# Kernel optimization log

Hardware: AMD Instinct MI355X
Metric: run time of the kernel (lower is better)

The kernel has to match this reference:

```python
import jax, jax.numpy as jnp
import numpy as np

MAX_DEG = 10
DEG_COUNTS = [10000, 130000, 170000, 160000, 100000, 15000, 5000, 2500, 2500, 2500, 2500]
DEG_STARTS = [int(s) for s in np.concatenate([[0], np.cumsum(DEG_COUNTS)[:-1]])]
N_ATOMS = int(sum(DEG_COUNTS))
BATCH = 24000
N_TASKS = 12
IN_FEAT = 75
CHANNELS = [IN_FEAT, 15, 20, 27, 36]


def setup_inputs() -> dict:
    key = jax.random.key(0)
    ks = jax.random.split(key, 32)
    inp = {}
    inp['atom_features'] = jax.random.normal(ks[0], (N_ATOMS, IN_FEAT), dtype=jnp.float32)
    # degree_slice[d] = (start, count) of atoms of degree d (atoms are sorted by degree)
    inp['degree_slice'] = jnp.array(np.stack([DEG_STARTS, DEG_COUNTS], axis=1), dtype=jnp.int32)
    inp['membership'] = jax.random.randint(ks[1], (N_ATOMS,), 0, BATCH, dtype=jnp.int32)
    for d in range(1, MAX_DEG + 1):
        inp[f'deg_adj_{d}'] = jax.random.randint(ks[1 + d], (DEG_COUNTS[d], d), 0, N_ATOMS, dtype=jnp.int32)
    for i in range(4):
        fi, fo = CHANNELS[i], CHANNELS[i + 1]
        inp[f'W{i+1}'] = (jax.random.normal(ks[12 + 2 * i], (2 * MAX_DEG + 1, fi, fo), dtype=jnp.float32)
                          / np.float32(np.sqrt(fi)))
        inp[f'b{i+1}'] = jnp.zeros((2 * MAX_DEG + 1, fo), dtype=jnp.float32)
    inp['W_dense'] = jax.random.normal(ks[30], (2 * CHANNELS[-1], N_TASKS * 2), dtype=jnp.float32) / np.float32(np.sqrt(2 * CHANNELS[-1]))
    inp['b_dense'] = jnp.zeros((N_TASKS * 2,), dtype=jnp.float32)
    return inp


def graph_conv(atoms, deg_adjs, W, b):
    # W: [2*MAX_DEG+1, in, out]; weight iterator order: (rel_d, self_d) for d=1..MAX_DEG, then self_0
    outs = [None] * (MAX_DEG + 1)
    for deg in range(1, MAX_DEG + 1):
        adj = deg_adjs[deg - 1]                      # [n_d, deg] neighbor indices
        rel = jnp.sum(atoms[adj], axis=1)            # gather + sum over neighbors -> [n_d, in]
        s, c = DEG_STARTS[deg], DEG_COUNTS[deg]
        self_atoms = atoms[s:s + c]                  # atoms of this degree (static slice)
        i = 2 * (deg - 1)
        outs[deg] = (rel @ W[i] + b[i]) + (self_atoms @ W[i + 1] + b[i + 1])
    outs[0] = atoms[:DEG_COUNTS[0]] @ W[2 * MAX_DEG] + b[2 * MAX_DEG]
    return jax.nn.selu(jnp.concatenate(outs, axis=0))


def graph_gather(atoms, membership):
    sums = jax.ops.segment_sum(atoms, membership, num_segments=BATCH)
    maxs = jax.ops.segment_max(atoms, membership, num_segments=BATCH)
    return jnp.tanh(jnp.concatenate([sums, maxs], axis=1))  # [BATCH, 2*36]


def reference(atom_features, degree_slice, membership,
              deg_adj_1, deg_adj_2, deg_adj_3, deg_adj_4, deg_adj_5,
              deg_adj_6, deg_adj_7, deg_adj_8, deg_adj_9, deg_adj_10,
              W1, b1, W2, b2, W3, b3, W4, b4, W_dense, b_dense):
    # degree_slice carries the same (start,count) info as the static DEG_STARTS/DEG_COUNTS.
    deg_adjs = [deg_adj_1, deg_adj_2, deg_adj_3, deg_adj_4, deg_adj_5,
                deg_adj_6, deg_adj_7, deg_adj_8, deg_adj_9, deg_adj_10]
    x = graph_conv(atom_features, deg_adjs, W1, b1)
    x = graph_conv(x, deg_adjs, W2, b2)
    x = graph_conv(x, deg_adjs, W3, b3)
    x = graph_conv(x, deg_adjs, W4, b4)
    mol = graph_gather(x, membership)                 # [BATCH, 72]
    logits = (mol @ W_dense + b_dense).reshape(BATCH, N_TASKS, 2)
    return jax.nn.softmax(logits, axis=-1)
```

## Files before the change

### kernel.cpp

```cpp
#include <hip/hip_runtime.h>
#include <hip/hip_fp16.h>
#include <cstdint>

#define NT 256
#define PT 128
#define N_ATOMS_C 600000
#define BATCH_C 24000

constexpr int K_COUNTS[11] = {10000,130000,170000,160000,100000,15000,5000,2500,2500,2500,2500};
constexpr int K_STARTS[11] = {0,10000,140000,310000,470000,570000,585000,590000,592500,595000,597500};
constexpr int DORD[11] = {10,9,8,7,6,5,4,3,2,1,0};

struct AdjPtrs { const int* p[10]; };

typedef _Float16 f16x8 __attribute__((ext_vector_type(8)));
typedef float f32x4 __attribute__((ext_vector_type(4)));

__device__ __forceinline__ float selu_f(float x) {
    const float scale = 1.0507009873554805f;
    const float alpha = 1.6732632423543772f;
    return scale * (x > 0.f ? x : alpha * expm1f(x));
}

__device__ __forceinline__ float2 up2(unsigned u) {
    const __half2 h = __builtin_bit_cast(__half2, u);
    return __half22float2(h);
}
__device__ __forceinline__ unsigned pack2(float a, float b) {
    const __half2 h = __float22half2_rn(make_float2(a, b));
    return __builtin_bit_cast(unsigned, h);
}

template<int NLD4>
__device__ __forceinline__ void load_row(const uint2* __restrict__ p, float* r) {
#pragma unroll
    for (int v = 0; v < NLD4; ++v) {
        const uint2 t = p[v];
        const float2 a = up2(t.x), b = up2(t.y);
        r[4*v] = a.x; r[4*v+1] = a.y; r[4*v+2] = b.x; r[4*v+3] = b.y;
    }
}
template<int NLD4>
__device__ __forceinline__ void add_row(const uint2* __restrict__ p, float* r) {
#pragma unroll
    for (int v = 0; v < NLD4; ++v) {
        const uint2 t = p[v];
        const float2 a = up2(t.x), b = up2(t.y);
        r[4*v] += a.x; r[4*v+1] += a.y; r[4*v+2] += b.x; r[4*v+3] += b.y;
    }
}
template<int NF, int FO>
__device__ __forceinline__ void fma_strip(const float* r, const float* __restrict__ w,
                                          float* acc) {
#pragma unroll
    for (int f = 0; f < NF; ++f)
#pragma unroll
        for (int o = 0; o < FO; ++o)
            acc[o] = fmaf(r[f], w[f * FO + o], acc[o]);
}

template<int TB>
__device__ __forceinline__ void blk2degT(int blk, int& deg, int& s, int& cnt, int& tile) {
    deg = 0; s = 0; cnt = 0; tile = 0;
#pragma unroll
    for (int di = 0; di < 11; ++di) {
        const int d = DORD[di];
        const int nb = (K_COUNTS[d] + TB - 1) / TB;
        if (blk < nb) { deg = d; s = K_STARTS[d]; cnt = K_COUNTS[d]; tile = blk; return; }
        blk -= nb;
    }
}

__global__ __launch_bounds__(128) void prep_kernel(
    const float* __restrict__ x0,
    const float* __restrict__ W,
    const float* __restrict__ bias,
    const int* __restrict__ mem,
    int* __restrict__ cnt,
    unsigned short* __restrict__ z,
    unsigned short* __restrict__ srow)
{
    __shared__ _Float16 sx[PT * 104];
    __shared__ _Float16 sb[80 * 104];

    int deg, s, c, tile;
    blk2degT<PT>(blockIdx.x, deg, s, c, tile);
    const int a0 = tile * PT;
    const int na = min(PT, c - a0);
    const int tid = threadIdx.x;
    const int wi_b = deg ? (2 * deg - 1) : 20;

    const float* src = x0 + (size_t)(s + a0) * 75;
    for (int i = tid; i < na * 75; i += PT) {
        const int j = i / 75, f = i - j * 75;
        sx[j * 104 + f] = (_Float16)src[i];
    }
    for (int i = tid; i < PT * 29; i += PT) {
        const int j = i / 29, f = 75 + (i - j * 29);
        sx[j * 104 + f] = (_Float16)0.f;
    }
    for (int i = tid; i < 80 * 104; i += PT) {
        const int col = i / 104, k = i - col * 104;
        const int p = col >> 4, o = col & 15;
        const int wi = (p < 4) ? 2 * p : wi_b;
        const float v = (k < 75 && o < 15) ? W[wi * 1125 + k * 15 + o] : 0.f;
        sb[col * 104 + k] = (_Float16)v;
    }
    __syncthreads();

    if (tid < na) atomicAdd(&cnt[mem[s + a0 + tid]], 1);

    const int lane = tid & 63, w = tid >> 6;
    const int lrow = lane & 15;
    const int kgrp = (lane >> 4) * 8;
    const int row0 = (lane >> 4) * 4;
    const int colo = lane & 15;

    float badd = 0.f;
    if (colo < 15)
        badd = bias[wi_b * 15 + colo] + (deg ? bias[2 * (deg - 1) * 15 + colo] : 0.f);

    f16x8 af[4][3];
#pragma unroll
    for (int mt = 0; mt < 4; ++mt)
#pragma unroll
        for (int ks = 0; ks < 3; ++ks)
            af[mt][ks] = *(const f16x8*)&sx[(w * 64 + mt * 16 + lrow) * 104 + ks * 32 + kgrp];

#pragma unroll
    for (int nt = 0; nt < 5; ++nt) {
        f16x8 bf[3];
#pragma unroll
        for (int ks = 0; ks < 3; ++ks)
            bf[ks] = *(const f16x8*)&sb[(nt * 16 + lrow) * 104 + ks * 32 + kgrp];
#pragma unroll
        for (int mt = 0; mt < 4; ++mt) {
            f32x4 acc = {0.f, 0.f, 0.f, 0.f};
#pragma unroll
            for (int ks = 0; ks < 3; ++ks)
                acc = __builtin_amdgcn_mfma_f32_16x16x32_f16(af[mt][ks], bf[ks], acc, 0, 0, 0);
#pragma unroll
            for (int reg = 0; reg < 4; ++reg) {
                const int ar = w * 64 + mt * 16 + row0 + reg;
                if (ar < na) {
                    const size_t atom = (size_t)(s + a0 + ar);
                    if (nt < 4) {
                        z[(size_t)nt * ((size_t)N_ATOMS_C * 16) + atom * 16 + colo] =
                            __builtin_bit_cast(unsigned short, (_Float16)acc[reg]);
                    } else {
                        const float v = (colo < 15) ? acc[reg] + badd : 0.f;
                        srow[atom * 16 + colo] =
                            __builtin_bit_cast(unsigned short, (_Float16)v);
                    }
                }
            }
        }
    }
}

__global__ __launch_bounds__(256) void conv1_kernel(
    const float* __restrict__ x0,
    const unsigned short* __restrict__ z,
    const unsigned short* __restrict__ srow,
    const float* __restrict__ W,
    AdjPtrs adjp,
    unsigned short* __restrict__ y1)
{
    int deg, s, c, tile;
    blk2degT<NT>(blockIdx.x, deg, s, c, tile);
    const int a = tile * NT + threadIdx.x;
    if (a >= c) return;
    const int atom = s + a;

    float acc[15];
    {
        const uint2* sp = reinterpret_cast<const uint2*>(srow + (size_t)atom * 16);
        float r[16];
        load_row<4>(sp, r);
#pragma unroll
        for (int o = 0; o < 15; ++o) acc[o] = r[o];
    }

    if (deg >= 1 && deg <= 4) {
        const unsigned short* zd = z + (size_t)(deg - 1) * ((size_t)N_ATOMS_C * 16);
        const int* ad = adjp.p[deg - 1] + (size_t)a * deg;
        int nb[4];
#pragma unroll
        for (int k = 0; k < 4; ++k) nb[k] = ad[k < deg ? k : 0];
        uint4 t[4][2];
#pragma unroll
        for (int k = 0; k < 4; ++k) {
            const uint4* p = reinterpret_cast<const uint4*>(zd + (size_t)nb[k] * 16);
            t[k][0] = p[0]; t[k][1] = p[1];
        }
#pragma unroll
        for (int k = 0; k < 4; ++k) {
            if (k < deg) {
                const unsigned w[8] = {t[k][0].x, t[k][0].y, t[k][0].z, t[k][0].w,
                                       t[k][1].x, t[k][1].y, t[k][1].z, t[k][1].w};
#pragma unroll
                for (int v = 0; v < 8; ++v) {
                    const float2 lo = up2(w[v]);
                    if (2 * v < 15)     acc[2 * v]     += lo.x;
                    if (2 * v + 1 < 15) acc[2 * v + 1] += lo.y;
                }
            }
        }
    } else if (deg >= 5) {
        const float* Wa = W + 2 * (deg - 1) * 1125;
        const int* ad = adjp.p[deg - 1] + (size_t)a * deg;
#pragma unroll 1
        for (int st = 0; st < 3; ++st) {
            float r[25];
#pragma unroll
            for (int j = 0; j < 25; ++j) r[j] = 0.f;
            for (int k = 0; k < deg; ++k) {
                const float* xr = x0 + (size_t)ad[k] * 75 + st * 25;
#pragma unroll
                for (int j = 0; j < 25; ++j) r[j] += xr[j];
            }
            fma_strip<25, 15>(r, Wa + st * 25 * 15, acc);
        }
    }

    uint2* yp = reinterpret_cast<uint2*>(y1 + (size_t)atom * 16);
    float o_[16];
#pragma unroll
    for (int o = 0; o < 16; ++o) o_[o] = (o < 15) ? selu_f(acc[o]) : 0.f;
    yp[0] = make_uint2(pack2(o_[0],o_[1]),  pack2(o_[2],o_[3]));
    yp[1] = make_uint2(pack2(o_[4],o_[5]),  pack2(o_[6],o_[7]));
    yp[2] = make_uint2(pack2(o_[8],o_[9]),  pack2(o_[10],o_[11]));
    yp[3] = make_uint2(pack2(o_[12],o_[13]),pack2(o_[14],o_[15]));
}

template<int FIN, int FINP, int FO, int FOP, int FS>
__global__ __launch_bounds__(256) void conv_kernel(
    const unsigned short* __restrict__ x,
    const float* __restrict__ W,
    const float* __restrict__ bias,
    AdjPtrs adjp,
    unsigned short* __restrict__ y)
{
    static_assert(FS % 4 == 0 && FINP % 4 == 0 && FOP % 4 == 0, "");
    constexpr int NSF = FIN / FS;
    constexpr int TF  = FIN - NSF * FS;
    constexpr int TLD4 = (TF + 3) / 4;
    static_assert(NSF * FS + TLD4 * 4 <= FINP, "tail reads past row");

    int deg, s, c, tile;
    blk2degT<NT>(blockIdx.x, deg, s, c, tile);
    const int a = tile * NT + threadIdx.x;
    if (a >= c) return;
    const int atom = s + a;

    const int wi_a = (deg == 0) ? 20 : 2 * (deg - 1);
    const int wi_b = (deg == 0) ? 20 : 2 * deg - 1;
    const float* Wa = W + wi_a * FIN * FO;
    const float* Wb = W + wi_b * FIN * FO;

    float acc[FO];
#pragma unroll
    for (int o = 0; o < FO; ++o)
        acc[o] = bias[wi_b * FO + o] + ((deg > 0) ? bias[wi_a * FO + o] : 0.f);

    const int* myadj = (deg > 0) ? (adjp.p[deg - 1] + (size_t)a * deg) : nullptr;
    const uint2* selfrow = reinterpret_cast<const uint2*>(x + (size_t)atom * FINP);

#pragma unroll 1
    for (int st = 0; st < NSF; ++st) {
        const int f0 = st * FS;
        float r[FS];
        load_row<FS / 4>(selfrow + (f0 >> 2), r);
        fma_strip<FS, FO>(r, Wb + f0 * FO, acc);
        if (deg > 0) {
#pragma unroll
            for (int f = 0; f < FS; ++f) r[f] = 0.f;
            for (int k = 0; k < deg; ++k)
                add_row<FS / 4>(reinterpret_cast<const uint2*>(
                    x + (size_t)myadj[k] * FINP) + (f0 >> 2), r);
            fma_strip<FS, FO>(r, Wa + f0 * FO, acc);
        }
    }
    if constexpr (TF > 0) {
        constexpr int f0 = NSF * FS;
        float r[TLD4 * 4];
        load_row<TLD4>(selfrow + (f0 >> 2), r);
        fma_strip<TF, FO>(r, Wb + f0 * FO, acc);
        if (deg > 0) {
#pragma unroll
            for (int f = 0; f < TLD4 * 4; ++f) r[f] = 0.f;
            for (int k = 0; k < deg; ++k)
                add_row<TLD4>(reinterpret_cast<const uint2*>(
                    x + (size_t)myadj[k] * FINP) + (f0 >> 2), r);
            fma_strip<TF, FO>(r, Wa + f0 * FO, acc);
        }
    }

    float outv[FOP];
#pragma unroll
    for (int o = 0; o < FOP; ++o) outv[o] = (o < FO) ? selu_f(acc[o]) : 0.f;
    uint2* yp = reinterpret_cast<uint2*>(y + (size_t)atom * FOP);
#pragma unroll
    for (int v = 0; v < FOP / 4; ++v)
        yp[v] = make_uint2(pack2(outv[4*v], outv[4*v+1]),
                           pack2(outv[4*v+2], outv[4*v+3]));
}

__global__ __launch_bounds__(256) void zero_cnt_kernel(int* __restrict__ cnt) {
    const int i = blockIdx.x * NT + threadIdx.x;
    if (i < BATCH_C) cnt[i] = 0;
}
__global__ __launch_bounds__(1024) void scan_kernel(const int* __restrict__ cnt,
                                                    int* __restrict__ base,
                                                    int* __restrict__ cursor) {
    __shared__ int part[1024];
    const int tid = threadIdx.x;
    constexpr int CH = 24;
    const int i0 = tid * CH;
    int sum = 0;
    for (int j = 0; j < CH; ++j) { const int i = i0 + j; if (i < BATCH_C) sum += cnt[i]; }
    part[tid] = sum;
    __syncthreads();
    for (int off = 1; off < 1024; off <<= 1) {
        const int v = (tid >= off) ? part[tid - off] : 0;
        __syncthreads(); part[tid] += v; __syncthreads();
    }
    int run = part[tid] - sum;
    for (int j = 0; j < CH; ++j) {
        const int i = i0 + j;
        if (i < BATCH_C) { base[i] = run; cursor[i] = run; run += cnt[i]; }
    }
    if (tid == 1023) base[BATCH_C] = part[1023];
}
__global__ __launch_bounds__(256) void scatter_kernel(const int* __restrict__ mem,
                                                      int* __restrict__ cursor,
                                                      int* __restrict__ alist) {
    const int i = blockIdx.x * NT + threadIdx.x;
    if (i < N_ATOMS_C) { const int p = atomicAdd(&cursor[mem[i]], 1); alist[p] = i; }
}

__global__ __launch_bounds__(256) void reduce_dense_kernel(
    const unsigned short* __restrict__ y4,
    const int* __restrict__ base, const int* __restrict__ alist,
    const float* __restrict__ Wd, const float* __restrict__ bd,
    float* __restrict__ out)
{
    __shared__ float sW[72 * 24];
    __shared__ float sb[24];
    __shared__ float molf[4][72];

    const int tid = threadIdx.x;
    for (int i = tid; i < 72 * 24; i += NT) sW[i] = Wd[i];
    if (tid < 24) sb[tid] = bd[tid];
    __syncthreads();

    const int w = tid >> 6, lane = tid & 63;
    const int mol = blockIdx.x * 4 + w;
    const int b0 = base[mol], b1 = base[mol + 1];

    if (lane < 36) {
        float s = 0.f, mx = -INFINITY;
        for (int k = b0; k < b1; ++k) {
            const int atom = alist[k];
            const float v = __half2float(__builtin_bit_cast(__half,
                                y4[(size_t)atom * 36 + lane]));
            s += v; mx = fmaxf(mx, v);
        }
        molf[w][lane] = tanhf(s);
        molf[w][36 + lane] = tanhf(mx);
    }
    __syncthreads();

    if (lane < 24) {
        float l = sb[lane];
#pragma unroll
        for (int f = 0; f < 72; ++f) l += molf[w][f] * sW[f * 24 + lane];
        const float lp = __shfl_xor(l, 1);
        const float m2 = fmaxf(l, lp);
        const float e = expf(l - m2), ep = expf(lp - m2);
        out[(size_t)mol * 24 + lane] = e / (e + ep);
    }
}

extern "C" void kernel_launch(void* const* d_in, const int* in_sizes, int n_in,
                              void* d_out, int out_size, void* d_ws, size_t ws_size,
                              hipStream_t stream)
{
    const float* x0         = (const float*)d_in[0];
    const int*   membership = (const int*)d_in[2];
    AdjPtrs adj;
    for (int d = 0; d < 10; ++d) adj.p[d] = (const int*)d_in[3 + d];
    const float *W1=(const float*)d_in[13], *b1=(const float*)d_in[14];
    const float *W2=(const float*)d_in[15], *b2=(const float*)d_in[16];
    const float *W3=(const float*)d_in[17], *b3=(const float*)d_in[18];
    const float *W4=(const float*)d_in[19], *b4=(const float*)d_in[20];
    const float *Wd=(const float*)d_in[21], *bd=(const float*)d_in[22];

    const size_t szA = 81600000;
    const size_t szB = 38400000;
    const size_t nInts = (size_t)N_ATOMS_C + (BATCH_C + 1) + BATCH_C + BATCH_C;
    if (ws_size < szA + szB + nInts * 4) return;

    char* base0 = (char*)d_ws;
    unsigned short* zbuf = (unsigned short*)base0;
    unsigned short* y2   = (unsigned short*)base0;
    unsigned short* y4   = (unsigned short*)(base0 + 38400000);
    unsigned short* srow = (unsigned short*)(base0 + szA);
    unsigned short* y1   = (unsigned short*)(base0 + szA + 19200000);
    unsigned short* y3   = (unsigned short*)(base0 + szA);
    int* alist  = (int*)(base0 + szA + szB);
    int* base   = alist + N_ATOMS_C;
    int* cursor = base + (BATCH_C + 1);
    int* cnt    = cursor + BATCH_C;

    int nblk = 0, nblkp = 0;
    for (int d = 0; d < 11; ++d) {
        nblk  += (K_COUNTS[d] + NT - 1) / NT;
        nblkp += (K_COUNTS[d] + PT - 1) / PT;
    }
    const int nb_atoms = (N_ATOMS_C + NT - 1) / NT;

    zero_cnt_kernel<<<(BATCH_C + NT - 1) / NT, NT, 0, stream>>>(cnt);
    prep_kernel<<<nblkp, PT, 0, stream>>>(x0, W1, b1, membership, cnt, zbuf, srow);
    scan_kernel<<<1, 1024, 0, stream>>>(cnt, base, cursor);
    scatter_kernel<<<nb_atoms, NT, 0, stream>>>(membership, cursor, alist);

    conv1_kernel<<<nblk, NT, 0, stream>>>(x0, zbuf, srow, W1, adj, y1);
    conv_kernel<15,16,20,32,16><<<nblk, NT, 0, stream>>>(y1, W2, b2, adj, y2);
    conv_kernel<20,32,27,32,32><<<nblk, NT, 0, stream>>>(y2, W3, b3, adj, y3);
    conv_kernel<27,32,36,36,32><<<nblk, NT, 0, stream>>>(y3, W4, b4, adj, y4);

    reduce_dense_kernel<<<BATCH_C / 4, NT, 0, stream>>>(y4, base, alist, Wd, bd, (float*)d_out);
}
```

Measured before the change: 605.5 us.

## Restructure prep kernel: 256 threads, vectorized loads, direct weight fragment loads

The prep kernel now runs 256 threads per 128-atom tile, with four waves each covering 32 rows instead of two waves covering 64. Input features are loaded as float4 vectors. Each lane now builds its MFMA B fragments straight from global weights instead of staging the weight panel in shared memory. This removes the per-block weight staging loop and a large LDS array, which should raise occupancy and shorten setup time. In exchange every wave reissues scalar, strided global weight loads, which mostly hit in cache.

```diff
diff --git a/kernel.cpp b/kernel.cpp
--- a/kernel.cpp
+++ b/kernel.cpp
@@ -3,7 +3,7 @@
 #include <cstdint>
 
 #define NT 256
-#define PT 128
+#define PA 128
 #define N_ATOMS_C 600000
 #define BATCH_C 24000
 
@@ -71,7 +71,7 @@
     }
 }
 
-__global__ __launch_bounds__(128) void prep_kernel(
+__global__ __launch_bounds__(256) void prep_kernel(
     const float* __restrict__ x0,
     const float* __restrict__ W,
     const float* __restrict__ bias,
@@ -80,31 +80,36 @@
     unsigned short* __restrict__ z,
     unsigned short* __restrict__ srow)
 {
-    __shared__ _Float16 sx[PT * 104];
-    __shared__ _Float16 sb[80 * 104];
+    __shared__ _Float16 sx[PA * 104];
 
     int deg, s, c, tile;
-    blk2degT<PT>(blockIdx.x, deg, s, c, tile);
-    const int a0 = tile * PT;
-    const int na = min(PT, c - a0);
+    blk2degT<PA>(blockIdx.x, deg, s, c, tile);
+    const int a0 = tile * PA;
+    const int na = min(PA, c - a0);
     const int tid = threadIdx.x;
     const int wi_b = deg ? (2 * deg - 1) : 20;
 
     const float* src = x0 + (size_t)(s + a0) * 75;
-    for (int i = tid; i < na * 75; i += PT) {
-        const int j = i / 75, f = i - j * 75;
-        sx[j * 104 + f] = (_Float16)src[i];
-    }
-    for (int i = tid; i < PT * 29; i += PT) {
+    const int flat = na * 75;
+    for (int i4 = tid; i4 * 4 < flat; i4 += NT) {
+        const int i = i4 * 4;
+        if (i + 4 <= flat) {
+            const f32x4 v = *reinterpret_cast<const f32x4*>(src + i);
+#pragma unroll
+            for (int e = 0; e < 4; ++e) {
+                const int j = (i + e) / 75, f = (i + e) - j * 75;
+                sx[j * 104 + f] = (_Float16)v[e];
+            }
+        } else {
+            for (int e = 0; i + e < flat; ++e) {
+                const int j = (i + e) / 75, f = (i + e) - j * 75;
+                sx[j * 104 + f] = (_Float16)src[i + e];
+            }
+        }
+    }
+    for (int i = tid; i < PA * 29; i += NT) {
         const int j = i / 29, f = 75 + (i - j * 29);
         sx[j * 104 + f] = (_Float16)0.f;
-    }
-    for (int i = tid; i < 80 * 104; i += PT) {
-        const int col = i / 104, k = i - col * 104;
-        const int p = col >> 4, o = col & 15;
-        const int wi = (p < 4) ? 2 * p : wi_b;
-        const float v = (k < 75 && o < 15) ? W[wi * 1125 + k * 15 + o] : 0.f;
-        sb[col * 104 + k] = (_Float16)v;
     }
     __syncthreads();
 
@@ -120,28 +125,37 @@
     if (colo < 15)
         badd = bias[wi_b * 15 + colo] + (deg ? bias[2 * (deg - 1) * 15 + colo] : 0.f);
 
-    f16x8 af[4][3];
-#pragma unroll
-    for (int mt = 0; mt < 4; ++mt)
+    f16x8 af[2][3];
+#pragma unroll
+    for (int mt = 0; mt < 2; ++mt)
 #pragma unroll
         for (int ks = 0; ks < 3; ++ks)
-            af[mt][ks] = *(const f16x8*)&sx[(w * 64 + mt * 16 + lrow) * 104 + ks * 32 + kgrp];
+            af[mt][ks] = *(const f16x8*)&sx[(w * 32 + mt * 16 + lrow) * 104 + ks * 32 + kgrp];
 
 #pragma unroll
     for (int nt = 0; nt < 5; ++nt) {
+        const int wi = (nt < 4) ? 2 * nt : wi_b;
+        const float* Wp = W + wi * 1125;
         f16x8 bf[3];
 #pragma unroll
-        for (int ks = 0; ks < 3; ++ks)
-            bf[ks] = *(const f16x8*)&sb[(nt * 16 + lrow) * 104 + ks * 32 + kgrp];
-#pragma unroll
-        for (int mt = 0; mt < 4; ++mt) {
+        for (int ks = 0; ks < 3; ++ks) {
+#pragma unroll
+            for (int j = 0; j < 8; ++j) {
+                const int k = ks * 32 + kgrp + j;
+                float v = 0.f;
+                if (k < 75 && lrow < 15) v = Wp[k * 15 + lrow];
+                bf[ks][j] = (_Float16)v;
+            }
+        }
+#pragma unroll
+        for (int mt = 0; mt < 2; ++mt) {
             f32x4 acc = {0.f, 0.f, 0.f, 0.f};
 #pragma unroll
             for (int ks = 0; ks < 3; ++ks)
                 acc = __builtin_amdgcn_mfma_f32_16x16x32_f16(af[mt][ks], bf[ks], acc, 0, 0, 0);
 #pragma unroll
             for (int reg = 0; reg < 4; ++reg) {
-                const int ar = w * 64 + mt * 16 + row0 + reg;
+                const int ar = w * 32 + mt * 16 + row0 + reg;
                 if (ar < na) {
                     const size_t atom = (size_t)(s + a0 + ar);
                     if (nt < 4) {
@@ -416,12 +430,12 @@
     int nblk = 0, nblkp = 0;
     for (int d = 0; d < 11; ++d) {
         nblk  += (K_COUNTS[d] + NT - 1) / NT;
-        nblkp += (K_COUNTS[d] + PT - 1) / PT;
+        nblkp += (K_COUNTS[d] + PA - 1) / PA;
     }
     const int nb_atoms = (N_ATOMS_C + NT - 1) / NT;
 
     zero_cnt_kernel<<<(BATCH_C + NT - 1) / NT, NT, 0, stream>>>(cnt);
-    prep_kernel<<<nblkp, PT, 0, stream>>>(x0, W1, b1, membership, cnt, zbuf, srow);
+    prep_kernel<<<nblkp, NT, 0, stream>>>(x0, W1, b1, membership, cnt, zbuf, srow);
     scan_kernel<<<1, 1024, 0, stream>>>(cnt, base, cursor);
     scatter_kernel<<<nb_atoms, NT, 0, stream>>>(membership, cursor, alist);
 
```

New measurement: 629.1 us. 3.9% more time.
